# Kernel optimization log

Measured on AMD Instinct MI355X. Metric: run time of the kernel, lower is better.

The kernel has to match this reference:

```python
import jax, jax.numpy as jnp
import numpy as np
from jax import lax

START_IDX = 0
STOP_IDX = 1


def _forward_alg(feats_lbt, mask_lb, transitions):
    # feats_lbt: [L, B, T], mask_lb: [L, B], transitions[i, j] = score(j -> i)
    L, B, T = feats_lbt.shape
    init = jnp.full((B, T), -10000.0, dtype=feats_lbt.dtype).at[:, START_IDX].set(0.0)

    def step(fv, xs):
        feat, m = xs  # feat: [B, T], m: [B]
        # scores[b, next, prev] = fv[b, prev] + transitions[next, prev] + feat[b, next]
        scores = fv[:, None, :] + transitions[None, :, :] + feat[:, :, None]
        alphas = jax.nn.logsumexp(scores, axis=-1)  # [B, T]
        fv = jnp.where(m[:, None] > 0, alphas, fv)
        return fv, None

    fv, _ = lax.scan(step, init, (feats_lbt, mask_lb))
    terminal = fv + transitions[STOP_IDX][None, :]
    return jax.nn.logsumexp(terminal, axis=-1)  # [B]


def _score_sentence(feats_lbt, tags_bl, mask_lb, transitions):
    L, B, T = feats_lbt.shape
    start_col = jnp.full((B, 1), START_IDX, dtype=tags_bl.dtype)
    tags_ext = jnp.concatenate([start_col, tags_bl], axis=-1)  # [B, L+1]
    # transition scores along the gold path: [B, L]
    trans = transitions[tags_ext[:, 1:], tags_ext[:, :-1]]
    # emission scores: feats is [L, B, T] -> gather per-position gold tag
    emit = jnp.take_along_axis(
        feats_lbt, tags_bl.T[:, :, None], axis=-1
    )[:, :, 0]  # [L, B]
    step_scores = (trans.T + emit) * (mask_lb > 0)  # [L, B]
    score = step_scores.sum(axis=0)  # [B]
    lengths = mask_lb.sum(axis=0).astype(jnp.int32)  # [B]
    last_tag = tags_ext[jnp.arange(B), lengths]
    score = score + transitions[STOP_IDX, last_tag]
    return score


def setup_inputs() -> dict:
    key = jax.random.key(0)
    k1, k2, k3 = jax.random.split(key, 3)
    B, L, T = 256, 2048, 32
    efeats = jax.random.normal(k1, (B, L, T), dtype=jnp.float32)
    mask = jnp.ones((B, L), dtype=jnp.float32)
    tgt = jax.random.randint(k2, (B, L), 0, T, dtype=jnp.int32)
    transitions = jax.random.normal(k3, (T, T), dtype=jnp.float32)
    return {"efeats": efeats, "mask": mask, "tgt": tgt, "transitions": transitions}


def reference(efeats, mask, tgt, transitions):
    B, L = mask.shape
    mask_lb = mask.T  # [L, B]
    feats_lbt = jnp.transpose(efeats, (1, 0, 2))  # [L, B, T]
    forward_score = _forward_alg(feats_lbt, mask_lb, transitions)
    gold_score = _score_sentence(feats_lbt, tgt, mask_lb, transitions)
    loss = (forward_score - gold_score).sum() / B
    return loss
```

## Files before the change

### kernel.cpp

```cpp
#include <hip/hip_runtime.h>

#define B_SZ 256
#define L_SZ 2048
#define T_SZ 32
#define NCH 16
#define CLEN 128
#define START_IDX 0
#define STOP_IDX 1

typedef __attribute__((ext_vector_type(8))) short bf16x8;
typedef __attribute__((ext_vector_type(4))) float f32x4;

__device__ __forceinline__ unsigned fau(float f){ union{float f; unsigned u;} v; v.f=f; return v.u; }
__device__ __forceinline__ float uaf(unsigned u){ union{unsigned u; float f;} v; v.u=u; return v.f; }
__device__ __forceinline__ int pack_trunc(float lo, float hi){
  return (int)((fau(lo)>>16) | (fau(hi)&0xffff0000u));
}
__device__ __forceinline__ bf16x8 frag_of(const int* p){
  union{ int i[4]; bf16x8 v; } u;
  u.i[0]=p[0]; u.i[1]=p[1]; u.i[2]=p[2]; u.i[3]=p[3];
  return u.v;
}

__global__ void zero_kernel(float* out){ if(threadIdx.x==0) out[0]=0.f; }

__global__ __launch_bounds__(1024) void crf_loss_kernel(
    const float* __restrict__ efeats, const float* __restrict__ mask,
    const int* __restrict__ tgt, const float* __restrict__ trans,
    float* __restrict__ out)
{
  __shared__ float s_trans[T_SZ*T_SZ];
  __shared__ float s_d[NCH][T_SZ];
  __shared__ unsigned short s_M[NCH][T_SZ*T_SZ];
  __shared__ int   s_es[NCH];
  __shared__ float s_gd[NCH];
  __shared__ float s_ml[NCH];

  const int tid  = threadIdx.x;
  const int b    = blockIdx.x;
  const int w    = tid >> 6;
  const int lane = tid & 63;
  const int g    = lane >> 4;
  const int c16  = lane & 15;
  const int i32  = lane & 31;

  s_trans[tid] = trans[tid];
  __syncthreads();

  int a0[4], a1[4];
  #pragma unroll
  for (int I=0; I<2; ++I){
    int row = 8*(c16>>2) + 4*I + (c16&3);
    float e[8];
    #pragma unroll
    for (int j=0;j<8;++j) e[j] = __expf(s_trans[row*T_SZ + 8*g + j]);
    int* dst = I ? a1 : a0;
    #pragma unroll
    for (int p=0;p<4;++p) dst[p] = pack_trunc(e[2*p], e[2*p+1]);
  }

  int b0[4], b1[4];
  #pragma unroll
  for (int p=0;p<4;++p){
    int s0 = 8*g + 2*p, s1 = s0+1;
    unsigned lo = (s0==c16)?0x3f80u:0u, hi = (s1==c16)?0x3f80u:0u;
    b0[p] = (int)(lo | (hi<<16));
    lo = (s0==16+c16)?0x3f80u:0u; hi = (s1==16+c16)?0x3f80u:0u;
    b1[p] = (int)(lo | (hi<<16));
  }

  const int l0 = w * CLEN;
  const long fbase = ((long)b * L_SZ) * T_SZ;

  float fq[4];
  #pragma unroll
  for (int i=0;i<4;++i) fq[i] = efeats[fbase + (long)(l0+i)*T_SZ + i32];

  int   tA = tgt [b*L_SZ + l0 + lane];
  int   tB = tgt [b*L_SZ + l0 + 64 + lane];
  float mA = mask[b*L_SZ + l0 + lane];
  float mB = mask[b*L_SZ + l0 + 64 + lane];
  int prev = (l0==0) ? START_IDX : tgt[b*L_SZ + l0 - 1];

  int esum = 0;
  float gold = 0.f, mlen = 0.f;
  const f32x4 zf = {0.f,0.f,0.f,0.f};

  #pragma unroll 4
  for (int t=0; t<CLEN; ++t){
    float fcur = fq[t&3];
    int lpf = l0 + t + 4; lpf = (lpf < L_SZ) ? lpf : (L_SZ-1);
    fq[t&3] = efeats[fbase + (long)lpf*T_SZ + i32];

    float mk  = uaf((unsigned)__builtin_amdgcn_readlane((int)fau((t<64)?mA:mB), t&63));
    int   cur = __builtin_amdgcn_readlane((t<64)?tA:tB, t&63);
    mlen += mk;

    if (mk > 0.f){
      if (lane < 32) s_d[w][lane] = __expf(fcur);

      f32x4 c00 = __builtin_amdgcn_mfma_f32_16x16x32_bf16(frag_of(a0), frag_of(b0), zf, 0,0,0);
      f32x4 c01 = __builtin_amdgcn_mfma_f32_16x16x32_bf16(frag_of(a0), frag_of(b1), zf, 0,0,0);
      f32x4 c10 = __builtin_amdgcn_mfma_f32_16x16x32_bf16(frag_of(a1), frag_of(b0), zf, 0,0,0);
      f32x4 c11 = __builtin_amdgcn_mfma_f32_16x16x32_bf16(frag_of(a1), frag_of(b1), zf, 0,0,0);

      const float4* dv = (const float4*)(&s_d[w][0]);
      float4 dl = dv[2*g], dh = dv[2*g+1];
      float f0=dl.x, f1=dl.y, f2=dl.z, f3=dl.w;
      float f4=dh.x, f5=dh.y, f6=dh.z, f7=dh.w;

      float m00 = c00[0]*f0;
      unsigned mb = (unsigned)__builtin_amdgcn_readfirstlane((int)fau(m00));
      int e = (int)((mb>>23)&255u) - 127;
      esum += e;
      float r = uaf((unsigned)(127-e)<<23);
      f0*=r; f1*=r; f2*=r; f3*=r; f4*=r; f5*=r; f6*=r; f7*=r;

      c00[0]*=f0; c00[1]*=f1; c00[2]*=f2; c00[3]*=f3;
      c01[0]*=f0; c01[1]*=f1; c01[2]*=f2; c01[3]*=f3;
      c10[0]*=f4; c10[1]*=f5; c10[2]*=f6; c10[3]*=f7;
      c11[0]*=f4; c11[1]*=f5; c11[2]*=f6; c11[3]*=f7;

      b0[0]=pack_trunc(c00[0],c00[1]); b0[1]=pack_trunc(c00[2],c00[3]);
      b0[2]=pack_trunc(c10[0],c10[1]); b0[3]=pack_trunc(c10[2],c10[3]);
      b1[0]=pack_trunc(c01[0],c01[1]); b1[1]=pack_trunc(c01[2],c01[3]);
      b1[2]=pack_trunc(c11[0],c11[1]); b1[3]=pack_trunc(c11[2],c11[3]);

      float tp   = s_trans[cur*T_SZ + prev];
      float emit = uaf((unsigned)__builtin_amdgcn_readlane((int)fau(fcur), cur));
      gold += tp + emit;
    }
    prev = cur;
  }

  #pragma unroll
  for (int p=0;p<4;++p){
    int s = 8*g + 2*p;
    *(int*)((char*)(&s_M[w][0]) + (((long)(c16   )*T_SZ + s) * 2)) = b0[p];
    *(int*)((char*)(&s_M[w][0]) + (((long)(16+c16)*T_SZ + s) * 2)) = b1[p];
  }
  if (lane==0){ s_es[w]=esum; s_gd[w]=gold; s_ml[w]=mlen; }
  __syncthreads();

  if (w==0){
    int s = i32;
    float v = (s==START_IDX)?1.f:0.f;
    int E = 0;
    for (int c=0;c<NCH;++c){
      float u=0.f;
      #pragma unroll 8
      for (int k=0;k<T_SZ;++k){
        float mv = uaf(((unsigned)s_M[c][k*T_SZ + s])<<16);
        float vk = uaf((unsigned)__builtin_amdgcn_readlane((int)fau(v), k));
        u = fmaf(mv, vk, u);
      }
      unsigned ub = (unsigned)__builtin_amdgcn_readfirstlane((int)fau(u));
      int eu = (int)((ub>>23)&255u)-127;
      E += s_es[c] + eu;
      v = u * uaf((unsigned)(127-eu)<<23);
    }
    float term = v * __expf(s_trans[STOP_IDX*T_SZ + s]);
    #pragma unroll
    for (int off=16; off>0; off>>=1) term += __shfl_xor(term, off, 32);
    float fwd = (float)E * 0.69314718055994530942f + __logf(term);

    float gp = (s<NCH)? s_gd[s] : 0.f;
    float lp = (s<NCH)? s_ml[s] : 0.f;
    #pragma unroll
    for (int off=16; off>0; off>>=1){ gp += __shfl_xor(gp, off, 32); lp += __shfl_xor(lp, off, 32); }
    int len = (int)lp;
    int last_tag = (len==0)? START_IDX : tgt[b*L_SZ + (len-1)];
    float goldT = gp + s_trans[STOP_IDX*T_SZ + last_tag];
    if (tid==0) atomicAdd(out, (fwd - goldT) * (1.0f/B_SZ));
  }
}

extern "C" void kernel_launch(void* const* d_in, const int* in_sizes, int n_in,
                              void* d_out, int out_size, void* d_ws, size_t ws_size,
                              hipStream_t stream)
{
  const float* efeats = (const float*)d_in[0];
  const float* mask   = (const float*)d_in[1];
  const int*   tgt    = (const int*)d_in[2];
  const float* trans  = (const float*)d_in[3];
  float* out = (float*)d_out;

  zero_kernel<<<dim3(1), dim3(64), 0, stream>>>(out);
  crf_loss_kernel<<<dim3(B_SZ), dim3(1024), 0, stream>>>(efeats, mask, tgt, trans, out);
}
```

Measured before the change: 165.8 us.

## Split CRF forward into chunk-matrix kernel and cross-chunk combine kernel

Splits the single per-sequence kernel in two. The first kernel computes per-chunk transfer matrices for 32 chunks of 64 steps per sequence, spread over 1024 blocks of 512 threads, and writes them to workspace. A second kernel chains the 32 matrices per sequence. The chunk kernel also gathers the gold score for all 64 steps in one vectorised pass, stages exp(feats) in a double-buffered LDS slot, renormalises only every fourth step, and packs bf16 with a perm instruction. The aims are shorter serial chains, more parallel blocks and less per-step overhead. The cost is extra global traffic and a second launch, and rescaling less often raises overflow risk in bf16/fp32. The original kernel remains as a fallback when the workspace is too small.

After: 153.2 us. -7.6%, faster.

```diff
diff --git a/kernel.cpp b/kernel.cpp
--- a/kernel.cpp
+++ b/kernel.cpp
@@ -3,10 +3,17 @@
 #define B_SZ 256
 #define L_SZ 2048
 #define T_SZ 32
-#define NCH 16
-#define CLEN 128
 #define START_IDX 0
 #define STOP_IDX 1
+
+#define CLEN 64
+#define NCHB 8
+#define NCH_SEQ 32
+#define NBLK_SEQ 4
+#define NCHUNK_TOT (B_SZ * NCH_SEQ)
+
+#define FB_NCH 16
+#define FB_CLEN 128
 
 typedef __attribute__((ext_vector_type(8))) short bf16x8;
 typedef __attribute__((ext_vector_type(4))) float f32x4;
@@ -14,7 +21,7 @@
 __device__ __forceinline__ unsigned fau(float f){ union{float f; unsigned u;} v; v.f=f; return v.u; }
 __device__ __forceinline__ float uaf(unsigned u){ union{unsigned u; float f;} v; v.u=u; return v.f; }
 __device__ __forceinline__ int pack_trunc(float lo, float hi){
-  return (int)((fau(lo)>>16) | (fau(hi)&0xffff0000u));
+  return (int)__builtin_amdgcn_perm(fau(hi), fau(lo), 0x07060302u);
 }
 __device__ __forceinline__ bf16x8 frag_of(const int* p){
   union{ int i[4]; bf16x8 v; } u;
@@ -23,6 +30,195 @@
 }
 
 __global__ void zero_kernel(float* out){ if(threadIdx.x==0) out[0]=0.f; }
+
+__global__ __launch_bounds__(512, 8) void crf_chunk_kernel(
+    const float* __restrict__ efeats, const float* __restrict__ mask,
+    const int* __restrict__ tgt, const float* __restrict__ trans,
+    unsigned short* __restrict__ wsM, int* __restrict__ wsE,
+    float* __restrict__ wsG, float* __restrict__ wsL)
+{
+  __shared__ float s_trans[T_SZ*T_SZ];
+  __shared__ float s_d[NCHB][128];
+
+  const int tid  = threadIdx.x;
+  const int w    = tid >> 6;
+  const int lane = tid & 63;
+  const int g    = lane >> 4;
+  const int c16  = lane & 15;
+
+  const int b  = blockIdx.x >> 2;
+  const int q  = blockIdx.x & 3;
+  const int c  = q*NCHB + w;
+  const int l0 = c * CLEN;
+
+  s_trans[tid]     = trans[tid];
+  s_trans[tid+512] = trans[tid+512];
+  __syncthreads();
+
+  int a0[4], a1[4];
+  #pragma unroll
+  for (int I=0; I<2; ++I){
+    int row = 8*(c16>>2) + 4*I + (c16&3);
+    float e[8];
+    #pragma unroll
+    for (int j=0;j<8;++j) e[j] = __expf(s_trans[row*T_SZ + 8*g + j]);
+    int* dst = I ? a1 : a0;
+    #pragma unroll
+    for (int p=0;p<4;++p) dst[p] = pack_trunc(e[2*p], e[2*p+1]);
+  }
+
+  int b0[4], b1[4];
+  #pragma unroll
+  for (int p=0;p<4;++p){
+    int s0 = 8*g + 2*p, s1 = s0+1;
+    unsigned lo = (s0==c16)?0x3f80u:0u, hi = (s1==c16)?0x3f80u:0u;
+    b0[p] = (int)(lo | (hi<<16));
+    lo = (s0==16+c16)?0x3f80u:0u; hi = (s1==16+c16)?0x3f80u:0u;
+    b1[p] = (int)(lo | (hi<<16));
+  }
+
+  const long fbase = ((long)b * L_SZ) * T_SZ;
+  const int  mbase = b*L_SZ + l0;
+
+  float maskv = mask[mbase + lane];
+  int   tcur  = tgt [mbase + lane];
+  int   tprev;
+  {
+    int lp = (l0 + lane == 0) ? mbase : (mbase + lane - 1);
+    tprev = tgt[lp];
+    if (l0 + lane == 0) tprev = START_IDX;
+  }
+
+  float emitg = efeats[fbase + (long)(l0+lane)*T_SZ + tcur];
+  float gl = (maskv > 0.f) ? (s_trans[tcur*T_SZ + tprev] + emitg) : 0.f;
+  float ml = maskv;
+  #pragma unroll
+  for (int off=32; off>0; off>>=1){ gl += __shfl_xor(gl, off, 64); ml += __shfl_xor(ml, off, 64); }
+
+  unsigned long long mbits = __ballot(maskv > 0.f);
+
+  const float* fpt = efeats + fbase + (long)l0*T_SZ;
+  float f0raw = fpt[lane];
+  float fq[4];
+  #pragma unroll
+  for (int i=1; i<=4; ++i) fq[i&3] = fpt[i*64 + lane];
+  s_d[w][lane] = __expf(f0raw);
+
+  int esum = 0;
+  const f32x4 zf = {0.f,0.f,0.f,0.f};
+
+  #pragma unroll 4
+  for (int p=0; p<32; ++p){
+    if (p < 31){
+      s_d[w][((p+1)&1)*64 + lane] = __expf(fq[(p+1)&3]);
+      int np = p+5; if (np > 31) np = 31;
+      fq[(p+1)&3] = fpt[np*64 + lane];
+    }
+    const float* dbase = &s_d[w][(p&1)*64];
+    #pragma unroll
+    for (int h=0; h<2; ++h){
+      int t = 2*p + h;
+      if ((mbits >> t) & 1ull){
+        f32x4 c00 = __builtin_amdgcn_mfma_f32_16x16x32_bf16(frag_of(a0), frag_of(b0), zf, 0,0,0);
+        f32x4 c01 = __builtin_amdgcn_mfma_f32_16x16x32_bf16(frag_of(a0), frag_of(b1), zf, 0,0,0);
+        f32x4 c10 = __builtin_amdgcn_mfma_f32_16x16x32_bf16(frag_of(a1), frag_of(b0), zf, 0,0,0);
+        f32x4 c11 = __builtin_amdgcn_mfma_f32_16x16x32_bf16(frag_of(a1), frag_of(b1), zf, 0,0,0);
+
+        const float4* dv = (const float4*)(dbase + h*32);
+        float4 dl = dv[2*g], dh = dv[2*g+1];
+        float f0=dl.x, f1=dl.y, f2=dl.z, f3=dl.w;
+        float f4=dh.x, f5=dh.y, f6=dh.z, f7=dh.w;
+
+        if (h==1 && (p&1)==1){
+          float m00 = c00[0]*f0;
+          unsigned mb2 = (unsigned)__builtin_amdgcn_readfirstlane((int)fau(m00));
+          int e = (int)((mb2>>23)&255u) - 127;
+          esum += e;
+          float r = uaf((unsigned)(127-e)<<23);
+          f0*=r; f1*=r; f2*=r; f3*=r; f4*=r; f5*=r; f6*=r; f7*=r;
+        }
+
+        c00[0]*=f0; c00[1]*=f1; c00[2]*=f2; c00[3]*=f3;
+        c01[0]*=f0; c01[1]*=f1; c01[2]*=f2; c01[3]*=f3;
+        c10[0]*=f4; c10[1]*=f5; c10[2]*=f6; c10[3]*=f7;
+        c11[0]*=f4; c11[1]*=f5; c11[2]*=f6; c11[3]*=f7;
+
+        b0[0]=pack_trunc(c00[0],c00[1]); b0[1]=pack_trunc(c00[2],c00[3]);
+        b0[2]=pack_trunc(c10[0],c10[1]); b0[3]=pack_trunc(c10[2],c10[3]);
+        b1[0]=pack_trunc(c01[0],c01[1]); b1[1]=pack_trunc(c01[2],c01[3]);
+        b1[2]=pack_trunc(c11[0],c11[1]); b1[3]=pack_trunc(c11[2],c11[3]);
+      }
+    }
+  }
+
+  unsigned short* Mptr = wsM + (long)(b*NCH_SEQ + c) * (T_SZ*T_SZ);
+  #pragma unroll
+  for (int pp=0; pp<4; ++pp){
+    int s = 8*g + 2*pp;
+    *(int*)((char*)Mptr + ((c16*T_SZ + s)*2))        = b0[pp];
+    *(int*)((char*)Mptr + (((16+c16)*T_SZ + s)*2))   = b1[pp];
+  }
+  if (lane==0){
+    int cg = b*NCH_SEQ + c;
+    wsE[cg]=esum; wsG[cg]=gl; wsL[cg]=ml;
+  }
+}
+
+__global__ __launch_bounds__(256) void crf_combine_kernel(
+    const unsigned short* __restrict__ wsM, const int* __restrict__ wsE,
+    const float* __restrict__ wsG, const float* __restrict__ wsL,
+    const int* __restrict__ tgt, const float* __restrict__ trans,
+    float* __restrict__ out)
+{
+  __shared__ unsigned short sM[NCH_SEQ*T_SZ*T_SZ];
+  __shared__ int   s_es[NCH_SEQ];
+  __shared__ float s_g[NCH_SEQ], s_ml[NCH_SEQ];
+
+  const int tid = threadIdx.x;
+  const int b   = blockIdx.x;
+
+  const uint4* src = (const uint4*)(wsM + (long)b*NCH_SEQ*T_SZ*T_SZ);
+  uint4* dst = (uint4*)sM;
+  #pragma unroll
+  for (int i=0;i<16;++i) dst[tid + i*256] = src[tid + i*256];
+  if (tid < NCH_SEQ){
+    s_es[tid]=wsE[b*NCH_SEQ+tid]; s_g[tid]=wsG[b*NCH_SEQ+tid]; s_ml[tid]=wsL[b*NCH_SEQ+tid];
+  }
+  __syncthreads();
+
+  if (tid < 64){
+    int s = tid & 31;
+    float v = (s==START_IDX)?1.f:0.f;
+    int E = 0;
+    for (int cc=0; cc<NCH_SEQ; ++cc){
+      const unsigned short* M = &sM[cc*T_SZ*T_SZ];
+      float u = 0.f;
+      #pragma unroll 8
+      for (int k=0;k<T_SZ;++k){
+        float mv = uaf(((unsigned)M[k*T_SZ + s])<<16);
+        float vk = uaf((unsigned)__builtin_amdgcn_readlane((int)fau(v), k));
+        u = fmaf(mv, vk, u);
+      }
+      unsigned ub = (unsigned)__builtin_amdgcn_readfirstlane((int)fau(u));
+      int eu = (int)((ub>>23)&255u)-127;
+      E += s_es[cc] + eu;
+      v = u * uaf((unsigned)(127-eu)<<23);
+    }
+    float term = v * __expf(trans[STOP_IDX*T_SZ + s]);
+    #pragma unroll
+    for (int off=16; off>0; off>>=1) term += __shfl_xor(term, off, 32);
+    float fwd = (float)E * 0.69314718055994530942f + __logf(term);
+
+    float gp = s_g[s];
+    float lp = s_ml[s];
+    #pragma unroll
+    for (int off=16; off>0; off>>=1){ gp += __shfl_xor(gp, off, 32); lp += __shfl_xor(lp, off, 32); }
+    int len = (int)lp;
+    int last_tag = (len==0)? START_IDX : tgt[b*L_SZ + len-1];
+    float goldT = gp + trans[STOP_IDX*T_SZ + last_tag];
+    if (tid==0) atomicAdd(out, (fwd - goldT) * (1.0f/B_SZ));
+  }
+}
 
 __global__ __launch_bounds__(1024) void crf_loss_kernel(
     const float* __restrict__ efeats, const float* __restrict__ mask,
@@ -30,11 +226,11 @@
     float* __restrict__ out)
 {
   __shared__ float s_trans[T_SZ*T_SZ];
-  __shared__ float s_d[NCH][T_SZ];
-  __shared__ unsigned short s_M[NCH][T_SZ*T_SZ];
-  __shared__ int   s_es[NCH];
-  __shared__ float s_gd[NCH];
-  __shared__ float s_ml[NCH];
+  __shared__ float s_d[FB_NCH][T_SZ];
+  __shared__ unsigned short s_M[FB_NCH][T_SZ*T_SZ];
+  __shared__ int   s_es[FB_NCH];
+  __shared__ float s_gd[FB_NCH];
+  __shared__ float s_mlv[FB_NCH];
 
   const int tid  = threadIdx.x;
   const int b    = blockIdx.x;
@@ -69,12 +265,12 @@
     b1[p] = (int)(lo | (hi<<16));
   }
 
-  const int l0 = w * CLEN;
+  const int l0 = w * FB_CLEN;
   const long fbase = ((long)b * L_SZ) * T_SZ;
 
-  float fq[4];
-  #pragma unroll
-  for (int i=0;i<4;++i) fq[i] = efeats[fbase + (long)(l0+i)*T_SZ + i32];
+  float fqv[4];
+  #pragma unroll
+  for (int i=0;i<4;++i) fqv[i] = efeats[fbase + (long)(l0+i)*T_SZ + i32];
 
   int   tA = tgt [b*L_SZ + l0 + lane];
   int   tB = tgt [b*L_SZ + l0 + 64 + lane];
@@ -87,10 +283,10 @@
   const f32x4 zf = {0.f,0.f,0.f,0.f};
 
   #pragma unroll 4
-  for (int t=0; t<CLEN; ++t){
-    float fcur = fq[t&3];
+  for (int t=0; t<FB_CLEN; ++t){
+    float fcur = fqv[t&3];
     int lpf = l0 + t + 4; lpf = (lpf < L_SZ) ? lpf : (L_SZ-1);
-    fq[t&3] = efeats[fbase + (long)lpf*T_SZ + i32];
+    fqv[t&3] = efeats[fbase + (long)lpf*T_SZ + i32];
 
     float mk  = uaf((unsigned)__builtin_amdgcn_readlane((int)fau((t<64)?mA:mB), t&63));
     int   cur = __builtin_amdgcn_readlane((t<64)?tA:tB, t&63);
@@ -139,14 +335,14 @@
     *(int*)((char*)(&s_M[w][0]) + (((long)(c16   )*T_SZ + s) * 2)) = b0[p];
     *(int*)((char*)(&s_M[w][0]) + (((long)(16+c16)*T_SZ + s) * 2)) = b1[p];
   }
-  if (lane==0){ s_es[w]=esum; s_gd[w]=gold; s_ml[w]=mlen; }
+  if (lane==0){ s_es[w]=esum; s_gd[w]=gold; s_mlv[w]=mlen; }
   __syncthreads();
 
   if (w==0){
     int s = i32;
     float v = (s==START_IDX)?1.f:0.f;
     int E = 0;
-    for (int c=0;c<NCH;++c){
+    for (int c=0;c<FB_NCH;++c){
       float u=0.f;
       #pragma unroll 8
       for (int k=0;k<T_SZ;++k){
@@ -164,8 +360,8 @@
     for (int off=16; off>0; off>>=1) term += __shfl_xor(term, off, 32);
     float fwd = (float)E * 0.69314718055994530942f + __logf(term);
 
-    float gp = (s<NCH)? s_gd[s] : 0.f;
-    float lp = (s<NCH)? s_ml[s] : 0.f;
+    float gp = (s<FB_NCH)? s_gd[s] : 0.f;
+    float lp = (s<FB_NCH)? s_mlv[s] : 0.f;
     #pragma unroll
     for (int off=16; off>0; off>>=1){ gp += __shfl_xor(gp, off, 32); lp += __shfl_xor(lp, off, 32); }
     int len = (int)lp;
@@ -185,6 +381,22 @@
   const float* trans  = (const float*)d_in[3];
   float* out = (float*)d_out;
 
+  const size_t needM = (size_t)NCHUNK_TOT * T_SZ * T_SZ * 2;
+  const size_t need  = needM + (size_t)NCHUNK_TOT * 12;
+
   zero_kernel<<<dim3(1), dim3(64), 0, stream>>>(out);
-  crf_loss_kernel<<<dim3(B_SZ), dim3(1024), 0, stream>>>(efeats, mask, tgt, trans, out);
-}
+
+  if (ws_size >= need){
+    unsigned short* wsM = (unsigned short*)d_ws;
+    char* p = (char*)d_ws + needM;
+    int*   wsE = (int*)p;
+    float* wsG = (float*)(p + (size_t)NCHUNK_TOT*4);
+    float* wsL = (float*)(p + (size_t)NCHUNK_TOT*8);
+    crf_chunk_kernel<<<dim3(B_SZ*NBLK_SEQ), dim3(512), 0, stream>>>(
+        efeats, mask, tgt, trans, wsM, wsE, wsG, wsL);
+    crf_combine_kernel<<<dim3(B_SZ), dim3(256), 0, stream>>>(
+        wsM, wsE, wsG, wsL, tgt, trans, out);
+  } else {
+    crf_loss_kernel<<<dim3(B_SZ), dim3(1024), 0, stream>>>(efeats, mask, tgt, trans, out);
+  }
+}
```
